# Performance work log

Measured on AMD Instinct MI355X. Metric: run time of the kernel, lower is better.

## Reference

```python
import jax, jax.numpy as jnp
import numpy as np

B, C, O, H, W = 16, 256, 256, 64, 64
T_DIM, E, K = 512, 4, 3


def setup_inputs() -> dict:
    key = jax.random.key(0)
    ks = jax.random.split(key, 12)
    def rn(k, shape, s=0.02):
        return jax.random.normal(k, shape, jnp.float32) * s
    return dict(
        x=jax.random.normal(ks[0], (B, C, H, W), jnp.float32),
        time_emb=jax.random.normal(ks[1], (B, T_DIM), jnp.float32),
        Wq=rn(ks[2], (C, T_DIM)), bq=jnp.zeros((C,), jnp.float32),
        Wk=rn(ks[3], (C, C)), bk=jnp.zeros((C,), jnp.float32),
        Wv=rn(ks[4], (C, C)), bv=jnp.zeros((C,), jnp.float32),
        Wm1=rn(ks[5], (C // 4, C)), bm1=jnp.zeros((C // 4,), jnp.float32),
        Wm2=rn(ks[6], (C, C // 4)), bm2=jnp.zeros((C,), jnp.float32),
        Wc=rn(ks[7], (E, C)), bc=jnp.zeros((E,), jnp.float32),
        expert_w=rn(ks[8], (E, O, C, K, K), s=0.05),  # [E, O, C_in/groups, K, K]
        expert_b=rn(ks[9], (E, O), s=0.05),
    )


def reference(x, time_emb, Wq, bq, Wk, bk, Wv, bv, Wm1, bm1, Wm2, bm2, Wc, bc, expert_w, expert_b):
    # --- router (eval mode: no gating noise) ---
    pooled = x.mean(axis=(2, 3))                      # [B, C] == avg_pool over full HxW
    q = time_emb @ Wq.T + bq                          # [B, C]
    k = pooled @ Wk.T + bk                            # [B, C]
    attn = jax.nn.sigmoid(q * k)
    v = pooled @ Wv.T + bv
    x_att = v * attn
    h = jax.nn.gelu(x_att @ Wm1.T + bm1, approximate=False) @ Wm2.T + bm2
    x_mix = x_att + h
    logits = x_mix @ Wc.T + bc                        # [B, E]
    rw = jnp.tanh(logits)                             # routing weights [B, E]

    # --- per-sample expert-weight mixing ---
    w_eff = jnp.einsum('be,eoihw->boihw', rw, expert_w)  # [B, O, C, K, K]
    b_eff = rw @ expert_b                                 # [B, O]

    # --- per-sample conv (equivalent to groups=B trick) ---
    def conv_one(xb, wb):
        # xb: [C, H, W], wb: [O, C, K, K]
        return jax.lax.conv_general_dilated(
            xb[None], wb, window_strides=(1, 1), padding=[(1, 1), (1, 1)],
            dimension_numbers=('NCHW', 'OIHW', 'NCHW'))[0]

    out = jax.vmap(conv_one)(x, w_eff)                 # [B, O, H, W]
    return out + b_eff[:, :, None, None]
```

## Files before the change

### kernel.cpp

```cpp
#include <hip/hip_runtime.h>

typedef __bf16 bf16x8 __attribute__((ext_vector_type(8)));
typedef float f32x4 __attribute__((ext_vector_type(4)));

__device__ __forceinline__ unsigned short f2bf(float f) {
  union { float f; unsigned int u; } v;
  v.f = f;
  unsigned int r = v.u + 0x7FFFu + ((v.u >> 16) & 1u);
  return (unsigned short)(r >> 16);
}

__device__ __forceinline__ void load_lds16(const void* g, void* l) {
  __builtin_amdgcn_global_load_lds(
      (__attribute__((address_space(1))) void*)(void*)g,
      (__attribute__((address_space(3))) void*)l, 16, 0, 0);
}

__global__ void transpose_kernel(const float* __restrict__ x, unsigned short* __restrict__ xTpad,
                                 float* __restrict__ part) {
  int bid = blockIdx.x;
  int b = bid / 66, hp = bid % 66;
  unsigned short* rowbase = xTpad + ((size_t)(b * 66 + hp)) * 66 * 256;
  int t = threadIdx.x;
  if (hp == 0 || hp == 65) {
    uint4 z = make_uint4(0u, 0u, 0u, 0u);
    for (int i = t; i < 2112; i += 256) ((uint4*)rowbase)[i] = z;
    return;
  }
  int h = hp - 1;
  __shared__ unsigned short lds[64][264];
  __shared__ float psum[256];
  const float* xb = x + ((size_t)b * 256 * 64 + h) * 64;
  int lane = t & 63;
  #pragma unroll
  for (int g = 0; g < 16; ++g) {
    int c = g * 16 + (t >> 4);
    int w0 = (t & 15) * 4;
    float4 v = *(const float4*)&xb[(size_t)c * 4096 + w0];
    lds[w0 + 0][c] = f2bf(v.x);
    lds[w0 + 1][c] = f2bf(v.y);
    lds[w0 + 2][c] = f2bf(v.z);
    lds[w0 + 3][c] = f2bf(v.w);
    float s = v.x + v.y + v.z + v.w;
    s += __shfl_xor(s, 1); s += __shfl_xor(s, 2);
    s += __shfl_xor(s, 4); s += __shfl_xor(s, 8);
    if ((lane & 15) == 0) psum[c] = s;
  }
  __syncthreads();
  #pragma unroll
  for (int p = 0; p < 8; ++p) {
    int w = p * 8 + (t >> 5);
    int seg = t & 31;
    uint4 u = *(const uint4*)&lds[w][seg * 8];
    *(uint4*)&rowbase[(w + 1) * 256 + seg * 8] = u;
  }
  if (t < 64) {
    uint4 z = make_uint4(0u, 0u, 0u, 0u);
    int row = (t >> 5) ? 65 : 0;
    *(uint4*)&rowbase[row * 256 + (t & 31) * 8] = z;
  }
  if (t < 256) part[((size_t)b * 64 + h) * 256 + t] = psum[t];
}

__global__ void router_kernel(
    const float* __restrict__ time_emb, const float* __restrict__ part,
    const float* __restrict__ Wq, const float* __restrict__ bq,
    const float* __restrict__ Wk, const float* __restrict__ bk,
    const float* __restrict__ Wv, const float* __restrict__ bv,
    const float* __restrict__ Wm1, const float* __restrict__ bm1,
    const float* __restrict__ Wm2, const float* __restrict__ bm2,
    const float* __restrict__ Wc, const float* __restrict__ bc,
    const float* __restrict__ expert_b,
    float* __restrict__ rw_out, float* __restrict__ beff_out) {
  int b = blockIdx.x, tid = threadIdx.x;
  int t = tid & 255;
  __shared__ float te[512], pl[256], qs[256], xa[256], m1s[64], xms[256], rws[4];
  te[tid] = time_emb[b * 512 + tid];
  if (tid < 256) {
    float s = 0.f;
    const float* pp = part + (size_t)b * 16384 + tid;
    for (int hh = 0; hh < 64; ++hh) s += pp[hh * 256];
    pl[tid] = s * (1.0f / 4096.0f);
  }
  __syncthreads();
  if (tid < 256) {
    float q = bq[t];
    const float4* wq4 = (const float4*)(Wq + (size_t)t * 512);
    #pragma unroll 4
    for (int i = 0; i < 128; ++i) {
      float4 w4 = wq4[i];
      q += w4.x * te[i*4] + w4.y * te[i*4+1] + w4.z * te[i*4+2] + w4.w * te[i*4+3];
    }
    qs[t] = q;
  } else {
    float k = bk[t], v = bv[t];
    const float4* wk4 = (const float4*)(Wk + (size_t)t * 256);
    const float4* wv4 = (const float4*)(Wv + (size_t)t * 256);
    #pragma unroll 4
    for (int i = 0; i < 64; ++i) {
      float4 a4 = wk4[i], b4 = wv4[i];
      float p0 = pl[i*4], p1 = pl[i*4+1], p2 = pl[i*4+2], p3 = pl[i*4+3];
      k += a4.x * p0 + a4.y * p1 + a4.z * p2 + a4.w * p3;
      v += b4.x * p0 + b4.y * p1 + b4.z * p2 + b4.w * p3;
    }
    xa[t] = k;
    xms[t] = v;
  }
  __syncthreads();
  if (tid < 256) {
    float k = xa[t], v = xms[t];
    float attn = 1.0f / (1.0f + expf(-(qs[t] * k)));
    qs[t] = v * attn;
  }
  __syncthreads();
  if (tid < 64) {
    float s = bm1[tid];
    const float4* w1 = (const float4*)(Wm1 + (size_t)tid * 256);
    #pragma unroll 4
    for (int i = 0; i < 64; ++i) {
      float4 w4 = w1[i];
      s += w4.x * qs[i*4] + w4.y * qs[i*4+1] + w4.z * qs[i*4+2] + w4.w * qs[i*4+3];
    }
    m1s[tid] = 0.5f * s * (1.0f + erff(s * 0.7071067811865476f));
  }
  __syncthreads();
  if (tid < 256) {
    float hsum = bm2[t];
    const float* w2 = Wm2 + (size_t)t * 64;
    for (int j = 0; j < 64; ++j) hsum += m1s[j] * w2[j];
    xms[t] = qs[t] + hsum;
  }
  __syncthreads();
  if (tid < 4) {
    float s = bc[tid];
    const float* wc = Wc + (size_t)tid * 256;
    for (int i = 0; i < 256; ++i) s += xms[i] * wc[i];
    float r = tanhf(s);
    rws[tid] = r;
    rw_out[b * 4 + tid] = r;
  }
  __syncthreads();
  if (tid < 256) {
    float be = 0.f;
    #pragma unroll
    for (int e = 0; e < 4; ++e) be += rws[e] * expert_b[e * 256 + t];
    beff_out[b * 256 + t] = be;
  }
}

__global__ __launch_bounds__(256, 1) void wmixT_kernel(
    const float* __restrict__ ew, const float* __restrict__ rw,
    unsigned short* __restrict__ wmixT) {
  int b = blockIdx.x >> 4, ob = blockIdx.x & 15;
  int t = threadIdx.x;
  __shared__ float lew[4][2304];
  __shared__ unsigned short obuf[288 * 128];
  float r0 = rw[b * 4 + 0], r1 = rw[b * 4 + 1], r2 = rw[b * 4 + 2], r3 = rw[b * 4 + 3];
  for (int op = 0; op < 16; ++op) {
    int o = ob * 16 + op;
    if (op) __syncthreads();
    #pragma unroll
    for (int e = 0; e < 4; ++e) {
      const float* s = ew + ((size_t)e * 256 + o) * 2304;
      #pragma unroll
      for (int j = 0; j < 9; ++j) lew[e][j * 256 + t] = s[j * 256 + t];
    }
    __syncthreads();
    int base = (t >> 3) * 128 + op * 8 + (t & 7);
    #pragma unroll
    for (int tt = 0; tt < 9; ++tt) {
      float m = r0 * lew[0][t * 9 + tt] + r1 * lew[1][t * 9 + tt] +
                r2 * lew[2][t * 9 + tt] + r3 * lew[3][t * 9 + tt];
      obuf[tt * 32 * 128 + base] = f2bf(m);
    }
  }
  __syncthreads();
  uint4* dst = (uint4*)(wmixT + (size_t)(b * 16 + ob) * 288 * 128);
  const uint4* src = (const uint4*)obuf;
  #pragma unroll
  for (int i = 0; i < 18; ++i) dst[i * 256 + t] = src[i * 256 + t];
}

__global__ __launch_bounds__(512, 2) void conv_kernel(
    const unsigned short* __restrict__ xT, const unsigned short* __restrict__ wmixT,
    const float* __restrict__ beff, float* __restrict__ out) {
  __shared__ unsigned short Bs[2][16384];
  int bid = blockIdx.x;
  int b = ((bid & 7) << 1) | ((bid >> 7) & 1);
  int nt = (bid >> 3) & 15;
  int h0 = nt << 2;
  int tid = threadIdx.x;
  int wid = tid >> 6, lane = tid & 63;
  int lm = lane & 15, lg = lane >> 4;
  int wm = wid >> 1, wn = wid & 1;

  const unsigned short* xTb = xT + (size_t)b * 66 * 66 * 256;
  const unsigned short* wmA = wmixT + (size_t)(b * 16 + wm * 4) * 288 * 128 + lane * 8;

  int lr = lane >> 3;
  int slot_g = (lane & 7) ^ lr;
  int b_lane = lr * 256 + slot_g * 8;

  int sw0 = ((0 + lg) ^ (lm & 7)) * 8;
  int sw1 = ((4 + lg) ^ (lm & 7)) * 8;

  auto stB = [&](int buf, int kh, int cc, int kw, int q) {
    const unsigned short* src =
        xTb + (size_t)((h0 + q + kh) * 66 + wid * 8 + kw) * 256 + cc * 64 + b_lane;
    load_lds16(src, &Bs[buf][(q * 64 + wid * 8) * 64]);
  };

  f32x4 acc[4][8];
  #pragma unroll
  for (int mf = 0; mf < 4; ++mf)
    #pragma unroll
    for (int nf = 0; nf < 8; ++nf)
      acc[mf][nf] = (f32x4){0.f, 0.f, 0.f, 0.f};

  bf16x8 Ae[4][2], Ao[4][2];

  stB(0, 0, 0, 0, 0); stB(0, 0, 0, 0, 1); stB(0, 0, 0, 0, 2); stB(0, 0, 0, 0, 3);
  __builtin_amdgcn_sched_barrier(0);
  #pragma unroll
  for (int mf = 0; mf < 4; ++mf)
    #pragma unroll
    for (int kk = 0; kk < 2; ++kk)
      Ae[mf][kk] = *(const bf16x8*)(wmA + (size_t)(mf * 288 + kk * 4) * 128);
  asm volatile("s_waitcnt vmcnt(8)" ::: "memory");
  __builtin_amdgcn_s_barrier();

  auto tile_body = [&](int t, int buf, bf16x8 (&Acur)[4][2], bf16x8 (&Anext)[4][2])
      __attribute__((always_inline)) {
    bool st = (t < 35);
    if (st) {
      int tn = t + 1;
      int khn = tn / 12, rn = tn % 12, ccn = rn / 3, kwn = rn % 3;
      stB(buf ^ 1, khn, ccn, kwn, 0); stB(buf ^ 1, khn, ccn, kwn, 1);
      stB(buf ^ 1, khn, ccn, kwn, 2); stB(buf ^ 1, khn, ccn, kwn, 3);
      __builtin_amdgcn_sched_barrier(0);
      int kbase = (khn * 3 + kwn) * 32 + ccn * 8;
      #pragma unroll
      for (int mf = 0; mf < 4; ++mf)
        #pragma unroll
        for (int kk = 0; kk < 2; ++kk)
          Anext[mf][kk] = *(const bf16x8*)(wmA + (size_t)(mf * 288 + kbase + kk * 4) * 128);
    }
    #pragma unroll
    for (int nf = 0; nf < 8; ++nf) {
      bf16x8 b0 = *(const bf16x8*)&Bs[buf][(wn * 128 + nf * 16 + lm) * 64 + sw0];
      bf16x8 b1 = *(const bf16x8*)&Bs[buf][(wn * 128 + nf * 16 + lm) * 64 + sw1];
      #pragma unroll
      for (int mf = 0; mf < 4; ++mf) {
        acc[mf][nf] = __builtin_amdgcn_mfma_f32_16x16x32_bf16(Acur[mf][0], b0, acc[mf][nf], 0, 0, 0);
        acc[mf][nf] = __builtin_amdgcn_mfma_f32_16x16x32_bf16(Acur[mf][1], b1, acc[mf][nf], 0, 0, 0);
      }
    }
    if (st) {
      asm volatile("s_waitcnt vmcnt(8)" ::: "memory");
      __builtin_amdgcn_s_barrier();
    }
  };

  for (int i = 0; i < 18; ++i) {
    tile_body(2 * i, 0, Ae, Ao);
    tile_body(2 * i + 1, 1, Ao, Ae);
  }

  #pragma unroll
  for (int mf = 0; mf < 4; ++mf) {
    int o = wm * 64 + mf * 16 + lg * 4;
    float be0 = beff[b * 256 + o + 0];
    float be1 = beff[b * 256 + o + 1];
    float be2 = beff[b * 256 + o + 2];
    float be3 = beff[b * 256 + o + 3];
    #pragma unroll
    for (int nf = 0; nf < 8; ++nf) {
      int n = wn * 128 + nf * 16 + lm;
      int hh = h0 + (n >> 6), w = n & 63;
      float* op = out + (((size_t)(b * 256 + o)) * 64 + hh) * 64 + w;
      op[0]            = acc[mf][nf][0] + be0;
      op[4096]         = acc[mf][nf][1] + be1;
      op[2 * 4096]     = acc[mf][nf][2] + be2;
      op[3 * 4096]     = acc[mf][nf][3] + be3;
    }
  }
}

extern "C" void kernel_launch(void* const* d_in, const int* in_sizes, int n_in,
                              void* d_out, int out_size, void* d_ws, size_t ws_size,
                              hipStream_t stream) {
  const float* x        = (const float*)d_in[0];
  const float* time_emb = (const float*)d_in[1];
  const float* Wq = (const float*)d_in[2];
  const float* bq = (const float*)d_in[3];
  const float* Wk = (const float*)d_in[4];
  const float* bk = (const float*)d_in[5];
  const float* Wv = (const float*)d_in[6];
  const float* bv = (const float*)d_in[7];
  const float* Wm1 = (const float*)d_in[8];
  const float* bm1 = (const float*)d_in[9];
  const float* Wm2 = (const float*)d_in[10];
  const float* bm2 = (const float*)d_in[11];
  const float* Wc = (const float*)d_in[12];
  const float* bc = (const float*)d_in[13];
  const float* expert_w = (const float*)d_in[14];
  const float* expert_b = (const float*)d_in[15];
  float* out = (float*)d_out;

  char* ws = (char*)d_ws;
  float* rw   = (float*)(ws + 0);
  float* beff = (float*)(ws + 1024);
  float* part = (float*)(ws + 20480);
  unsigned short* xTpad = (unsigned short*)(ws + 1069056);
  unsigned short* wmixT = (unsigned short*)(ws + 1069056 + 35684352);

  transpose_kernel<<<1056, 256, 0, stream>>>(x, xTpad, part);
  router_kernel<<<16, 512, 0, stream>>>(time_emb, part, Wq, bq, Wk, bk, Wv, bv,
                                        Wm1, bm1, Wm2, bm2, Wc, bc, expert_b, rw, beff);
  wmixT_kernel<<<256, 256, 0, stream>>>(expert_w, rw, wmixT);
  conv_kernel<<<256, 512, 0, stream>>>(xTpad, wmixT, beff, out);
}
```

Measured before the change: 155.1 us.

## Reuse input halo tile across conv taps and stage weights through LDS

The conv kernel now loads each 64-channel input chunk once, as a 6-row by 66-column halo tile, into a swizzled LDS buffer and reuses it for all nine taps. Previously the input was re-staged from global memory for every tap. Weights are now double-buffered into LDS with async loads instead of being read per lane from global, and the weight-mixing kernel pads its output buffer to reduce bank conflicts. The router's pooling reduction is split across eight accumulators. LDS use per block grows to about 114 KB, so launch bounds drop to one block per SM, and each tap now waits for all memory loads to finish, which reduces latency hiding.

```diff
diff --git a/kernel.cpp b/kernel.cpp
--- a/kernel.cpp
+++ b/kernel.cpp
@@ -77,10 +77,17 @@
   __shared__ float te[512], pl[256], qs[256], xa[256], m1s[64], xms[256], rws[4];
   te[tid] = time_emb[b * 512 + tid];
   if (tid < 256) {
-    float s = 0.f;
     const float* pp = part + (size_t)b * 16384 + tid;
-    for (int hh = 0; hh < 64; ++hh) s += pp[hh * 256];
-    pl[tid] = s * (1.0f / 4096.0f);
+    float s0 = 0.f, s1 = 0.f, s2 = 0.f, s3 = 0.f,
+          s4 = 0.f, s5 = 0.f, s6 = 0.f, s7 = 0.f;
+    #pragma unroll
+    for (int hh = 0; hh < 64; hh += 8) {
+      s0 += pp[(hh + 0) * 256]; s1 += pp[(hh + 1) * 256];
+      s2 += pp[(hh + 2) * 256]; s3 += pp[(hh + 3) * 256];
+      s4 += pp[(hh + 4) * 256]; s5 += pp[(hh + 5) * 256];
+      s6 += pp[(hh + 6) * 256]; s7 += pp[(hh + 7) * 256];
+    }
+    pl[tid] = (((s0 + s1) + (s2 + s3)) + ((s4 + s5) + (s6 + s7))) * (1.0f / 4096.0f);
   }
   __syncthreads();
   if (tid < 256) {
@@ -154,7 +161,7 @@
   int b = blockIdx.x >> 4, ob = blockIdx.x & 15;
   int t = threadIdx.x;
   __shared__ float lew[4][2304];
-  __shared__ unsigned short obuf[288 * 128];
+  __shared__ unsigned short obuf[288 * 136];
   float r0 = rw[b * 4 + 0], r1 = rw[b * 4 + 1], r2 = rw[b * 4 + 2], r3 = rw[b * 4 + 3];
   for (int op = 0; op < 16; ++op) {
     int o = ob * 16 + op;
@@ -166,25 +173,29 @@
       for (int j = 0; j < 9; ++j) lew[e][j * 256 + t] = s[j * 256 + t];
     }
     __syncthreads();
-    int base = (t >> 3) * 128 + op * 8 + (t & 7);
+    int base = (t >> 3) * 136 + op * 8 + (t & 7);
     #pragma unroll
     for (int tt = 0; tt < 9; ++tt) {
       float m = r0 * lew[0][t * 9 + tt] + r1 * lew[1][t * 9 + tt] +
                 r2 * lew[2][t * 9 + tt] + r3 * lew[3][t * 9 + tt];
-      obuf[tt * 32 * 128 + base] = f2bf(m);
-    }
-  }
-  __syncthreads();
-  uint4* dst = (uint4*)(wmixT + (size_t)(b * 16 + ob) * 288 * 128);
-  const uint4* src = (const uint4*)obuf;
-  #pragma unroll
-  for (int i = 0; i < 18; ++i) dst[i * 256 + t] = src[i * 256 + t];
-}
-
-__global__ __launch_bounds__(512, 2) void conv_kernel(
+      obuf[tt * 4352 + base] = f2bf(m);
+    }
+  }
+  __syncthreads();
+  unsigned short* dst = wmixT + (size_t)(b * 16 + ob) * 36864;
+  #pragma unroll
+  for (int i = 0; i < 18; ++i) {
+    int flat = i * 256 + t;
+    int row = flat >> 4, q = flat & 15;
+    *(uint4*)&dst[flat * 8] = *(const uint4*)&obuf[row * 136 + q * 8];
+  }
+}
+
+__global__ __launch_bounds__(512, 1) void conv_kernel(
     const unsigned short* __restrict__ xT, const unsigned short* __restrict__ wmixT,
     const float* __restrict__ beff, float* __restrict__ out) {
-  __shared__ unsigned short Bs[2][16384];
+  __shared__ unsigned short As[2][16384];
+  __shared__ unsigned short Ch[25344];
   int bid = blockIdx.x;
   int b = ((bid & 7) << 1) | ((bid >> 7) & 1);
   int nt = (bid >> 3) & 15;
@@ -195,20 +206,64 @@
   int wm = wid >> 1, wn = wid & 1;
 
   const unsigned short* xTb = xT + (size_t)b * 66 * 66 * 256;
-  const unsigned short* wmA = wmixT + (size_t)(b * 16 + wm * 4) * 288 * 128 + lane * 8;
-
-  int lr = lane >> 3;
-  int slot_g = (lane & 7) ^ lr;
-  int b_lane = lr * 256 + slot_g * 8;
-
-  int sw0 = ((0 + lg) ^ (lm & 7)) * 8;
-  int sw1 = ((4 + lg) ^ (lm & 7)) * 8;
-
-  auto stB = [&](int buf, int kh, int cc, int kw, int q) {
-    const unsigned short* src =
-        xTb + (size_t)((h0 + q + kh) * 66 + wid * 8 + kw) * 256 + cc * 64 + b_lane;
-    load_lds16(src, &Bs[buf][(q * 64 + wid * 8) * 64]);
+  const unsigned short* wmTb = wmixT + (size_t)b * 16 * 36864;
+
+  const unsigned short* srcA[4];
+  #pragma unroll
+  for (int r = 0; r < 4; ++r) {
+    int u = r * 4096 + tid * 8;
+    srcA[r] = wmTb + (size_t)(u >> 10) * 36864 + (u & 1023);
+  }
+  auto stageA = [&](int buf, int koff) {
+    #pragma unroll
+    for (int r = 0; r < 4; ++r)
+      load_lds16(srcA[r] + koff * 128, &As[buf][r * 4096 + tid * 8]);
   };
+
+  int csoff[7], cdoff[7];
+  #pragma unroll
+  for (int r = 0; r < 7; ++r) {
+    int f = (r < 6) ? (r * 4096 + tid * 8) : (24576 + tid * 8);
+    int row = f / 4224;
+    int rem = f - row * 4224;
+    int w = rem >> 6, cs = rem & 63;
+    csoff[r] = ((h0 + row) * 66 + w) * 256 + cs;
+    cdoff[r] = row * 4224 + (w << 6) + (cs ^ ((w & 7) << 3));
+  }
+  uint4 creg0, creg1, creg2, creg3, creg4, creg5, cregT;
+  auto loadChunk = [&](int cc) {
+    creg0 = *(const uint4*)(xTb + csoff[0] + cc * 64);
+    creg1 = *(const uint4*)(xTb + csoff[1] + cc * 64);
+    creg2 = *(const uint4*)(xTb + csoff[2] + cc * 64);
+    creg3 = *(const uint4*)(xTb + csoff[3] + cc * 64);
+    creg4 = *(const uint4*)(xTb + csoff[4] + cc * 64);
+    creg5 = *(const uint4*)(xTb + csoff[5] + cc * 64);
+    if (tid < 96) cregT = *(const uint4*)(xTb + csoff[6] + cc * 64);
+  };
+  auto writeChunk = [&]() {
+    *(uint4*)&Ch[cdoff[0]] = creg0;
+    *(uint4*)&Ch[cdoff[1]] = creg1;
+    *(uint4*)&Ch[cdoff[2]] = creg2;
+    *(uint4*)&Ch[cdoff[3]] = creg3;
+    *(uint4*)&Ch[cdoff[4]] = creg4;
+    *(uint4*)&Ch[cdoff[5]] = creg5;
+    if (tid < 96) *(uint4*)&Ch[cdoff[6]] = cregT;
+  };
+
+  int aoff[4][2];
+  #pragma unroll
+  for (int mf = 0; mf < 4; ++mf)
+    #pragma unroll
+    for (int kk = 0; kk < 2; ++kk)
+      aoff[mf][kk] = (wm * 4 + mf) * 1024 + (kk * 4 + lg) * 128 + lm * 8;
+  int nbase[8], wv8[8];
+  #pragma unroll
+  for (int nf = 0; nf < 8; ++nf) {
+    int n = wn * 128 + nf * 16 + lm;
+    int hq = n >> 6, w = n & 63;
+    nbase[nf] = hq * 4224 + w * 64;
+    wv8[nf] = w;
+  }
 
   f32x4 acc[4][8];
   #pragma unroll
@@ -217,53 +272,52 @@
     for (int nf = 0; nf < 8; ++nf)
       acc[mf][nf] = (f32x4){0.f, 0.f, 0.f, 0.f};
 
-  bf16x8 Ae[4][2], Ao[4][2];
-
-  stB(0, 0, 0, 0, 0); stB(0, 0, 0, 0, 1); stB(0, 0, 0, 0, 2); stB(0, 0, 0, 0, 3);
-  __builtin_amdgcn_sched_barrier(0);
-  #pragma unroll
-  for (int mf = 0; mf < 4; ++mf)
-    #pragma unroll
-    for (int kk = 0; kk < 2; ++kk)
-      Ae[mf][kk] = *(const bf16x8*)(wmA + (size_t)(mf * 288 + kk * 4) * 128);
-  asm volatile("s_waitcnt vmcnt(8)" ::: "memory");
+  loadChunk(0);
+  stageA(0, 0);
+  asm volatile("s_waitcnt vmcnt(0)" ::: "memory");
+  writeChunk();
+  asm volatile("s_waitcnt lgkmcnt(0)" ::: "memory");
   __builtin_amdgcn_s_barrier();
 
-  auto tile_body = [&](int t, int buf, bf16x8 (&Acur)[4][2], bf16x8 (&Anext)[4][2])
-      __attribute__((always_inline)) {
-    bool st = (t < 35);
-    if (st) {
-      int tn = t + 1;
-      int khn = tn / 12, rn = tn % 12, ccn = rn / 3, kwn = rn % 3;
-      stB(buf ^ 1, khn, ccn, kwn, 0); stB(buf ^ 1, khn, ccn, kwn, 1);
-      stB(buf ^ 1, khn, ccn, kwn, 2); stB(buf ^ 1, khn, ccn, kwn, 3);
+  for (int cc = 0; cc < 4; ++cc) {
+    #pragma unroll
+    for (int tap = 0; tap < 9; ++tap) {
+      const int kh = tap / 3, kw = tap % 3;
+      int abuf = (cc + tap) & 1;
+      bool last = (cc == 3 && tap == 8);
+      if (!last) {
+        int koff_next = (tap < 8) ? ((tap + 1) * 32 + cc * 8) : ((cc + 1) * 8);
+        stageA(abuf ^ 1, koff_next);
+      }
+      if (tap == 0 && cc < 3) loadChunk(cc + 1);
       __builtin_amdgcn_sched_barrier(0);
-      int kbase = (khn * 3 + kwn) * 32 + ccn * 8;
+      bf16x8 af[4][2];
       #pragma unroll
       for (int mf = 0; mf < 4; ++mf)
         #pragma unroll
         for (int kk = 0; kk < 2; ++kk)
-          Anext[mf][kk] = *(const bf16x8*)(wmA + (size_t)(mf * 288 + kbase + kk * 4) * 128);
-    }
-    #pragma unroll
-    for (int nf = 0; nf < 8; ++nf) {
-      bf16x8 b0 = *(const bf16x8*)&Bs[buf][(wn * 128 + nf * 16 + lm) * 64 + sw0];
-      bf16x8 b1 = *(const bf16x8*)&Bs[buf][(wn * 128 + nf * 16 + lm) * 64 + sw1];
+          af[mf][kk] = *(const bf16x8*)&As[abuf][aoff[mf][kk]];
       #pragma unroll
-      for (int mf = 0; mf < 4; ++mf) {
-        acc[mf][nf] = __builtin_amdgcn_mfma_f32_16x16x32_bf16(Acur[mf][0], b0, acc[mf][nf], 0, 0, 0);
-        acc[mf][nf] = __builtin_amdgcn_mfma_f32_16x16x32_bf16(Acur[mf][1], b1, acc[mf][nf], 0, 0, 0);
+      for (int nf = 0; nf < 8; ++nf) {
+        int wp7 = (wv8[nf] + kw) & 7;
+        int ba = nbase[nf] + kh * 4224 + kw * 64 + ((lg ^ wp7) << 3);
+        bf16x8 b0 = *(const bf16x8*)&Ch[ba];
+        bf16x8 b1 = *(const bf16x8*)&Ch[ba ^ 32];
+        #pragma unroll
+        for (int mf = 0; mf < 4; ++mf) {
+          acc[mf][nf] = __builtin_amdgcn_mfma_f32_16x16x32_bf16(af[mf][0], b0, acc[mf][nf], 0, 0, 0);
+          acc[mf][nf] = __builtin_amdgcn_mfma_f32_16x16x32_bf16(af[mf][1], b1, acc[mf][nf], 0, 0, 0);
+        }
       }
-    }
-    if (st) {
-      asm volatile("s_waitcnt vmcnt(8)" ::: "memory");
+      __builtin_amdgcn_sched_barrier(0);
+      asm volatile("s_waitcnt vmcnt(0)" ::: "memory");
       __builtin_amdgcn_s_barrier();
-    }
-  };
-
-  for (int i = 0; i < 18; ++i) {
-    tile_body(2 * i, 0, Ae, Ao);
-    tile_body(2 * i + 1, 1, Ao, Ae);
+      if (tap == 8 && cc < 3) {
+        writeChunk();
+        asm volatile("s_waitcnt lgkmcnt(0)" ::: "memory");
+        __builtin_amdgcn_s_barrier();
+      }
+    }
   }
 
   #pragma unroll
```

New measurement: 295.3 us. 90.4% more time.
